# Kernel optimization log

Hardware: AMD Instinct MI355X
Metric: run time of the kernel (lower is better)

The kernel has to match this reference:

```python
import jax, jax.numpy as jnp
import numpy as np

B, S, H = 2, 2048, 2048
E, K, HID = 8, 2, 4096          # num_experts, top-k, expert hidden (2*H)
NH, HD = 8, 256                  # attention heads, head_dim
MS, MD = 256, 512                # memory_size, memory_dim
RSTEPS, RD = 3, 512              # reasoning steps, reasoning_dim
SCALE = 16.0                     # sqrt(head_dim)


def setup_inputs() -> dict:
    key = jax.random.key(0)
    ks = iter(jax.random.split(key, 64))
    def w(shape, s=0.02):
        return (jax.random.normal(next(ks), shape, jnp.float32) * s)
    z = lambda *shape: jnp.zeros(shape, jnp.float32)
    inp = {
        'hidden_states': jax.random.normal(next(ks), (B, S, H), jnp.float32),
        'attention_mask': jnp.zeros((B, S), jnp.float32),  # 0 = unmasked (faithful: mask*-1e9 added)
        # MoE
        'gate_w': w((H, E)), 'gate_b': z(E),
        'moe_w1': w((E, H, HID)), 'moe_b1': z(E, HID),
        'moe_w2': w((E, HID, H)), 'moe_b2': z(E, H),
        # memory-augmented attention
        'q_w': w((H, H)), 'q_b': z(H),
        'k_w': w((H, H)), 'k_b': z(H),
        'v_w': w((H, H)), 'v_b': z(H),
        'o_w': w((H, H)), 'o_b': z(H),
        'mem_values': jax.random.normal(next(ks), (MS, MD), jnp.float32),
        'mem_proj_w': w((MD, H)), 'mem_proj_b': z(H),
        'mem_attn_w': w((H, MS)), 'mem_attn_b': z(MS),
        # hierarchical reasoning (stacked over steps)
        'rs_w1': w((RSTEPS, H, RD)), 'rs_b1': z(RSTEPS, RD),
        'rs_w2': w((RSTEPS, RD, H)), 'rs_b2': z(RSTEPS, H),
        'ln_g': jnp.ones((RSTEPS, H), jnp.float32), 'ln_b': z(RSTEPS, H),
        'hg_w1': w((RSTEPS, H, H // 4)), 'hg_b1': z(RSTEPS, H // 4),
        'hg_w2': w((RSTEPS, H // 4, 1)), 'hg_b2': z(RSTEPS, 1),
        'integ_w': w((RSTEPS * H, H)), 'integ_b': z(H),
    }
    return inp


def _layernorm(x, g, b, eps=1e-5):
    m = x.mean(-1, keepdims=True)
    v = ((x - m) ** 2).mean(-1, keepdims=True)
    return (x - m) / jnp.sqrt(v + eps) * g + b


def _forward(hidden_states, attention_mask, gate_w, gate_b, moe_w1, moe_b1, moe_w2, moe_b2,
             q_w, q_b, k_w, k_b, v_w, v_b, o_w, o_b, mem_values, mem_proj_w, mem_proj_b,
             mem_attn_w, mem_attn_b, rs_w1, rs_b1, rs_w2, rs_b2, ln_g, ln_b,
             hg_w1, hg_b1, hg_w2, hg_b2, integ_w, integ_b):
    h = hidden_states
    N = B * S
    # ---- Mixture of Experts (top-k routing, dense combine-weight formulation) ----
    x_flat = h.reshape(N, H)
    gate_probs = jax.nn.softmax(x_flat @ gate_w + gate_b, axis=-1)        # [N,E]
    topk_s, topk_i = jax.lax.top_k(gate_probs, K)                          # [N,K]
    topk_p = jax.nn.softmax(topk_s, axis=-1)                               # renormalize over top-k
    comb = jnp.zeros((N, E), x_flat.dtype).at[jnp.arange(N)[:, None], topk_i].add(topk_p)
    h1 = jax.nn.relu(jnp.einsum('nd,edh->neh', x_flat, moe_w1) + moe_b1)   # [N,E,HID]
    eo = jnp.einsum('neh,ehd->ned', h1, moe_w2) + moe_b2                   # [N,E,H]
    moe_out = jnp.einsum('ned,ne->nd', eo, comb).reshape(B, S, H)
    h = h + 0.5 * moe_out
    # ---- Memory-augmented attention ----
    q = (h @ q_w + q_b).reshape(B, S, NH, HD).transpose(0, 2, 1, 3)
    k = (h @ k_w + k_b).reshape(B, S, NH, HD).transpose(0, 2, 1, 3)
    v = (h @ v_w + v_b).reshape(B, S, NH, HD).transpose(0, 2, 1, 3)
    scores = jnp.einsum('bhqd,bhkd->bhqk', q, k) / SCALE
    scores = scores + attention_mask[:, None, None, :] * (-1e9)
    probs = jax.nn.softmax(scores, axis=-1)
    attn = jnp.einsum('bhqk,bhkd->bhqd', probs, v).transpose(0, 2, 1, 3).reshape(B, S, H)
    mem_p = jax.nn.softmax(h @ mem_attn_w + mem_attn_b, axis=-1)           # [B,S,MS]
    mem_o = (mem_p @ mem_values) @ mem_proj_w + mem_proj_b                 # [B,S,H]
    mem_out = (attn + 0.3 * mem_o) @ o_w + o_b
    h = h + mem_out
    # ---- Hierarchical reasoning ----
    cur = h
    outs = []
    for i in range(RSTEPS):
        so = jax.nn.relu(cur @ rs_w1[i] + rs_b1[i]) @ rs_w2[i] + rs_b2[i]
        so = _layernorm(so, ln_g[i], ln_b[i])
        g = jax.nn.sigmoid(jax.nn.relu(cur @ hg_w1[i] + hg_b1[i]) @ hg_w2[i] + hg_b2[i])  # [B,S,1]
        cur = cur + g * so
        outs.append(cur)
    final = jnp.concatenate(outs, axis=-1) @ integ_w + integ_b
    return h + final


def reference(hidden_states, attention_mask, gate_w, gate_b, moe_w1, moe_b1, moe_w2, moe_b2,
              q_w, q_b, k_w, k_b, v_w, v_b, o_w, o_b, mem_values, mem_proj_w, mem_proj_b,
              mem_attn_w, mem_attn_b, rs_w1, rs_b1, rs_w2, rs_b2, ln_g, ln_b,
              hg_w1, hg_b1, hg_w2, hg_b2, integ_w, integ_b):
    return _forward(hidden_states, attention_mask, gate_w, gate_b, moe_w1, moe_b1, moe_w2, moe_b2,
                    q_w, q_b, k_w, k_b, v_w, v_b, o_w, o_b, mem_values, mem_proj_w, mem_proj_b,
                    mem_attn_w, mem_attn_b, rs_w1, rs_b1, rs_w2, rs_b2, ln_g, ln_b,
                    hg_w1, hg_b1, hg_w2, hg_b2, integ_w, integ_b)
```

## Files before the change

### kernel.cpp

```cpp
#include <hip/hip_runtime.h>
#include <string.h>


typedef __attribute__((ext_vector_type(4))) float f32x4;
typedef __attribute__((ext_vector_type(8))) __bf16 bf16x8;

#define NTOK 4096
#define HDIM 2048
#define AS1 __attribute__((address_space(1)))
#define AS3 __attribute__((address_space(3)))

__device__ __forceinline__ unsigned short f2bf(float f) {
  unsigned u = __float_as_uint(f);
  unsigned r = (u + 0x7fffu + ((u >> 16) & 1u)) >> 16;
  return (unsigned short)r;
}
__device__ __forceinline__ float bf2f(unsigned short u) {
  return __uint_as_float(((unsigned)u) << 16);
}
__device__ __forceinline__ void unpack8(uint4 r, float* v) {
  v[0]=bf2f((unsigned short)(r.x&0xffff)); v[1]=bf2f((unsigned short)(r.x>>16));
  v[2]=bf2f((unsigned short)(r.y&0xffff)); v[3]=bf2f((unsigned short)(r.y>>16));
  v[4]=bf2f((unsigned short)(r.z&0xffff)); v[5]=bf2f((unsigned short)(r.z>>16));
  v[6]=bf2f((unsigned short)(r.w&0xffff)); v[7]=bf2f((unsigned short)(r.w>>16));
}
__device__ __forceinline__ uint4 pack8(const float* v) {
  uint4 r;
  r.x = (unsigned)f2bf(v[0]) | ((unsigned)f2bf(v[1])<<16);
  r.y = (unsigned)f2bf(v[2]) | ((unsigned)f2bf(v[3])<<16);
  r.z = (unsigned)f2bf(v[4]) | ((unsigned)f2bf(v[5])<<16);
  r.w = (unsigned)f2bf(v[6]) | ((unsigned)f2bf(v[7])<<16);
  return r;
}

__global__ void k_tconv(const float* __restrict__ in, unsigned short* __restrict__ out,
                        int R, int C, long inB, long outB) {
  __shared__ float tl[32][33];
  const int z = blockIdx.z;
  const float* ip = in + (long)z * inB;
  unsigned short* op = out + (long)z * outB;
  const int tx = threadIdx.x & 31, ty = threadIdx.x >> 5;
  const int c0 = blockIdx.x * 32, r0 = blockIdx.y * 32;
#pragma unroll
  for (int i = 0; i < 4; i++)
    tl[ty + i*8][tx] = ip[(long)(r0 + ty + i*8) * C + c0 + tx];
  __syncthreads();
#pragma unroll
  for (int i = 0; i < 4; i++)
    op[(long)(c0 + ty + i*8) * R + r0 + tx] = f2bf(tl[tx][ty + i*8]);
}

__global__ void k_cvt(const float* __restrict__ in, unsigned short* __restrict__ out, long n4) {
  long i = (long)blockIdx.x * blockDim.x + threadIdx.x;
  if (i < n4) {
    float4 v = ((const float4*)in)[i];
    float vv[4] = {v.x, v.y, v.z, v.w};
    union { unsigned short u[4]; uint2 d; } p;
#pragma unroll
    for (int j = 0; j < 4; j++) p.u[j] = f2bf(vv[j]);
    ((uint2*)out)[i] = p.d;
  }
}

__global__ void k_tvact(const unsigned short* __restrict__ qkv, unsigned short* __restrict__ vT) {
  __shared__ unsigned short tl[32][33];
  const int z = blockIdx.z, b = z >> 3, hh = z & 7;
  const unsigned short* ip = qkv + (long)b * 2048 * 6144 + 4096 + hh * 256;
  unsigned short* op = vT + (long)z * 256 * 2048;
  const int tx = threadIdx.x & 31, ty = threadIdx.x >> 5;
  const int d0 = blockIdx.x * 32, s0 = blockIdx.y * 32;
#pragma unroll
  for (int i = 0; i < 4; i++)
    tl[ty + i*8][tx] = ip[(long)(s0 + ty + i*8) * 6144 + d0 + tx];
  __syncthreads();
#pragma unroll
  for (int i = 0; i < 4; i++)
    op[(long)(d0 + ty + i*8) * 2048 + s0 + tx] = tl[tx][ty + i*8];
}

__global__ void k_maskvec(const float* __restrict__ m, float* __restrict__ mv) {
  int i = blockIdx.x * 256 + threadIdx.x;
  if (i < 4096) mv[i] = -1e9f * m[i];
}

__global__ void k_zero(int* p) { if (threadIdx.x < 8) p[threadIdx.x] = 0; }

__global__ void k_cat3(const float* __restrict__ a, const float* __restrict__ b,
                       const float* __restrict__ c, float* __restrict__ o) {
  int i = blockIdx.x * 256 + threadIdx.x;
  if (i < 2048) { o[i] = a[i]; o[2048 + i] = b[i]; o[4096 + i] = c[i]; }
}

__global__ void k_cat2x3(const float* __restrict__ a, const float* __restrict__ b,
                         float* __restrict__ o) {
  int i = blockIdx.x * 256 + threadIdx.x;
  if (i < 1536) { int s = i >> 9, c = i & 511; o[s * 1024 + c] = a[i]; o[s * 1024 + 512 + c] = b[i]; }
}

__global__ void k_gate(const float* __restrict__ x, const float* __restrict__ gw,
                       const float* __restrict__ gb, int* __restrict__ meta,
                       int* __restrict__ e0a, int* __restrict__ e1a,
                       float* __restrict__ w0a, float* __restrict__ w1a) {
  const int wv = threadIdx.x >> 6, ln = threadIdx.x & 63;
  const int n = blockIdx.x * 4 + wv;
  const float* xr = x + (long)n * HDIM;
  float s[8] = {0,0,0,0,0,0,0,0};
  for (int k = ln; k < HDIM; k += 64) {
    float xv = xr[k];
    const float* g = gw + (long)k * 8;
#pragma unroll
    for (int e = 0; e < 8; e++) s[e] += xv * g[e];
  }
#pragma unroll
  for (int e = 0; e < 8; e++)
    for (int d = 32; d; d >>= 1) s[e] += __shfl_xor(s[e], d);
  if (ln == 0) {
    float mx = -1e30f;
#pragma unroll
    for (int e = 0; e < 8; e++) { s[e] += gb[e]; mx = fmaxf(mx, s[e]); }
    float p[8], sum = 0.f;
#pragma unroll
    for (int e = 0; e < 8; e++) { p[e] = expf(s[e] - mx); sum += p[e]; }
    float inv = 1.f / sum;
#pragma unroll
    for (int e = 0; e < 8; e++) p[e] *= inv;
    int e0 = 0;
    for (int e = 1; e < 8; e++) if (p[e] > p[e0]) e0 = e;
    int e1 = (e0 == 0) ? 1 : 0;
    for (int e = 0; e < 8; e++) if (e != e0 && p[e] > p[e1]) e1 = e;
    float q = expf(p[e1] - p[e0]);
    float w0 = 1.f / (1.f + q), w1 = q / (1.f + q);
    e0a[n] = e0; e1a[n] = e1; w0a[n] = w0; w1a[n] = w1;
    atomicAdd(&meta[e0], 1); atomicAdd(&meta[e1], 1);
  }
}

__global__ void k_buildmap(int* meta) {
  if (threadIdx.x == 0 && blockIdx.x == 0) {
    int cum = 0, nT = 0;
    for (int e = 0; e < 8; e++) {
      int c = meta[e];
      meta[16 + e] = cum; meta[24 + e] = cum + c; meta[8 + e] = 0;
      int t = (c + 127) >> 7;
      for (int i = 0; i < t; i++) { meta[33 + nT] = e; meta[129 + nT] = cum + i * 128; nT++; }
      cum += c;
    }
    meta[32] = nT;
  }
}

__global__ void k_scatter(int* __restrict__ meta, const int* __restrict__ e0a,
                          const int* __restrict__ e1a, int* __restrict__ s0a,
                          int* __restrict__ s1a, int* __restrict__ srcTok) {
  const int n = blockIdx.x * 256 + threadIdx.x;
  if (n < NTOK) {
    int e0 = e0a[n], e1 = e1a[n];
    int s0 = meta[16 + e0] + atomicAdd(&meta[8 + e0], 1);
    int s1 = meta[16 + e1] + atomicAdd(&meta[8 + e1], 1);
    s0a[n] = s0; s1a[n] = s1; srcTok[s0] = n; srcTok[s1] = n;
  }
}

__global__ void k_gather(const unsigned short* __restrict__ xb, const int* __restrict__ srcTok,
                         unsigned short* __restrict__ xg) {
  const int r = blockIdx.x;
  int n = srcTok[r]; if (n < 0 || n >= NTOK) n = 0;
  ((uint4*)(xg + (long)r * HDIM))[threadIdx.x] =
      ((const uint4*)(xb + (long)n * HDIM))[threadIdx.x];
}

__global__ void k_combine(const float* __restrict__ h, const unsigned short* __restrict__ eo,
                          const int* __restrict__ s0a, const int* __restrict__ s1a,
                          const float* __restrict__ w0a, const float* __restrict__ w1a,
                          float* __restrict__ h2, unsigned short* __restrict__ h2b) {
  const int n = blockIdx.x, c = threadIdx.x * 8;
  const float w0 = w0a[n], w1 = w1a[n];
  uint4 a = *(const uint4*)(eo + (long)s0a[n] * HDIM + c);
  uint4 b = *(const uint4*)(eo + (long)s1a[n] * HDIM + c);
  float va[8], vb[8]; unpack8(a, va); unpack8(b, vb);
  const float* hr = h + (long)n * HDIM + c;
  float o[8];
#pragma unroll
  for (int j = 0; j < 8; j++) o[j] = hr[j] + 0.5f * (w0 * va[j] + w1 * vb[j]);
  float* h2r = h2 + (long)n * HDIM + c;
#pragma unroll
  for (int j = 0; j < 8; j++) h2r[j] = o[j];
  *(uint4*)(h2b + (long)n * HDIM + c) = pack8(o);
}

__global__ void k_softmax2048(unsigned short* __restrict__ p) {
  const long r = blockIdx.x;
  unsigned short* row = p + r * 2048;
  const int t = threadIdx.x, wv = t >> 6, ln = t & 63;
  uint4 raw = ((const uint4*)row)[t];
  float v[8]; unpack8(raw, v);
  float m = v[0];
#pragma unroll
  for (int j = 1; j < 8; j++) m = fmaxf(m, v[j]);
  for (int d = 32; d; d >>= 1) m = fmaxf(m, __shfl_xor(m, d));
  __shared__ float sm[4], ssum[4];
  if (ln == 0) sm[wv] = m;
  __syncthreads();
  m = fmaxf(fmaxf(sm[0], sm[1]), fmaxf(sm[2], sm[3]));
  float s = 0.f;
#pragma unroll
  for (int j = 0; j < 8; j++) { v[j] = expf(v[j] - m); s += v[j]; }
  for (int d = 32; d; d >>= 1) s += __shfl_xor(s, d);
  if (ln == 0) ssum[wv] = s;
  __syncthreads();
  s = ssum[0] + ssum[1] + ssum[2] + ssum[3];
  const float inv = 1.f / s;
#pragma unroll
  for (int j = 0; j < 8; j++) v[j] *= inv;
  ((uint4*)row)[t] = pack8(v);
}

__global__ void k_softmax256(const float* __restrict__ in, unsigned short* __restrict__ out) {
  const int wv = threadIdx.x >> 6, ln = threadIdx.x & 63;
  const long r = (long)blockIdx.x * 4 + wv;
  const float4 v4 = ((const float4*)(in + r * 256))[ln];
  float v[4] = {v4.x, v4.y, v4.z, v4.w};
  float m = fmaxf(fmaxf(v[0], v[1]), fmaxf(v[2], v[3]));
  for (int d = 32; d; d >>= 1) m = fmaxf(m, __shfl_xor(m, d));
  float s = 0.f;
#pragma unroll
  for (int j = 0; j < 4; j++) { v[j] = expf(v[j] - m); s += v[j]; }
  for (int d = 32; d; d >>= 1) s += __shfl_xor(s, d);
  const float inv = 1.f / s;
  union { unsigned short u[4]; uint2 d2; } p;
#pragma unroll
  for (int j = 0; j < 4; j++) p.u[j] = f2bf(v[j] * inv);
  ((uint2*)(out + r * 256))[ln] = p.d2;
}

__global__ void k_gdot(const unsigned short* __restrict__ g1, long ld, const float* __restrict__ w,
                       const float* __restrict__ bb, float* __restrict__ gv) {
  const int wv = threadIdx.x >> 6, ln = threadIdx.x & 63;
  const int n = blockIdx.x * 4 + wv;
  uint4 raw = *(const uint4*)(g1 + (long)n * ld + ln * 8);
  float v[8]; unpack8(raw, v);
  const float4 wa = ((const float4*)w)[ln * 2];
  const float4 wb = ((const float4*)w)[ln * 2 + 1];
  float s = v[0]*wa.x + v[1]*wa.y + v[2]*wa.z + v[3]*wa.w
          + v[4]*wb.x + v[5]*wb.y + v[6]*wb.z + v[7]*wb.w;
  for (int d = 32; d; d >>= 1) s += __shfl_xor(s, d);
  if (ln == 0) gv[n] = 1.f / (1.f + expf(-(s + bb[0])));
}

__global__ void k_lnupdate(const float* __restrict__ so, const float* __restrict__ curIn,
                           const float* __restrict__ gv, const float* __restrict__ lng,
                           const float* __restrict__ lnb, float* __restrict__ curOut,
                           unsigned short* __restrict__ curbOut, unsigned short* __restrict__ outs,
                           int step) {
  const int n = blockIdx.x, t = threadIdx.x, wv = t >> 6, ln = t & 63, c = t * 8;
  const float* row = so + (long)n * 2048 + c;
  float x[8];
#pragma unroll
  for (int j = 0; j < 8; j++) x[j] = row[j];
  float s1 = 0.f, s2 = 0.f;
#pragma unroll
  for (int j = 0; j < 8; j++) { s1 += x[j]; s2 += x[j] * x[j]; }
  for (int d = 32; d; d >>= 1) { s1 += __shfl_xor(s1, d); s2 += __shfl_xor(s2, d); }
  __shared__ float a1[4], a2[4];
  if (ln == 0) { a1[wv] = s1; a2[wv] = s2; }
  __syncthreads();
  s1 = a1[0] + a1[1] + a1[2] + a1[3];
  s2 = a2[0] + a2[1] + a2[2] + a2[3];
  const float mean = s1 * (1.f / 2048.f);
  const float var = s2 * (1.f / 2048.f) - mean * mean;
  const float rstd = rsqrtf(var + 1e-5f);
  const float g = gv[n];
  const float* ci = curIn + (long)n * 2048 + c;
  float o[8];
#pragma unroll
  for (int j = 0; j < 8; j++) {
    float l = (x[j] - mean) * rstd * lng[c + j] + lnb[c + j];
    o[j] = ci[j] + g * l;
  }
  float* co = curOut + (long)n * 2048 + c;
#pragma unroll
  for (int j = 0; j < 8; j++) co[j] = o[j];
  *(uint4*)(curbOut + (long)n * 2048 + c) = pack8(o);
  *(uint4*)(outs + (long)n * 6144 + (long)step * 2048 + c) = pack8(o);
}

struct GArgs {
  const unsigned short* A; long lda, aSO, aSI;
  const unsigned short* Bt; long ldb, bSO, bSI;
  int M, N, K;
  const float* adv; long advSO, advSI;
  float alpha, rscale;
  const float* rF; long ldrF, rfSO, rfSI;
  const unsigned short* rB; long ldrB, rbSO, rbSI;
  float* oF; long ldoF, ofSO, ofSI;
  unsigned short* oB; long ldoB, obSO, obSI;
  const int* meta;
};

template <int MOE, int RELU, int RESID, int OUTF, int OUTB>
__global__ __launch_bounds__(512) void gemm_bt(GArgs g) {
  __shared__ unsigned short lds[2 * 16384];
  const int t = threadIdx.x, wv = t >> 6, ln = t & 63, ln15 = ln & 15;
  const int lr8 = ln >> 3;
  const int lsl = (ln & 7) ^ lr8;
  const int bz = blockIdx.z;
  int row0, rowMax;
  const unsigned short *A, *Bt;
  long advO = 0, rFO = 0, rBO = 0, oFO = 0, oBO = 0;
  if constexpr (MOE) {
    const int ty = blockIdx.y;
    if (ty >= g.meta[32]) return;
    const int e = g.meta[33 + ty];
    row0 = g.meta[129 + ty]; rowMax = g.meta[24 + e];
    A = g.A; Bt = g.Bt + (long)e * g.bSO;
    advO = (long)e * g.advSO;
  } else {
    row0 = blockIdx.y << 7; rowMax = g.M;
    const long bo = (long)(bz >> 3), bi = (long)(bz & 7);
    A = g.A + bo * g.aSO + bi * g.aSI;
    Bt = g.Bt + bo * g.bSO + bi * g.bSI;
    advO = bo * g.advSO + bi * g.advSI;
    rFO = bo * g.rfSO + bi * g.rfSI;
    rBO = bo * g.rbSO + bi * g.rbSI;
    oFO = bo * g.ofSO + bi * g.ofSI;
    oBO = bo * g.obSO + bi * g.obSI;
  }
  const int col0 = blockIdx.x << 7;
  const long lda = g.lda, ldb = g.ldb;
  const int wm = (wv >> 2) << 6;
  const int wc = (wv & 3) << 5;

  auto STAGE = [&](int kt, unsigned base) {
    const long kk = ((long)kt << 6) + (lsl << 3);
#pragma unroll
    for (int l = 0; l < 2; ++l) {
      const int rb = (wv << 4) + (l << 3);
      int gr = row0 + rb + lr8;
      if constexpr (MOE) gr = (gr < rowMax) ? gr : (rowMax - 1);
      __builtin_amdgcn_global_load_lds(
          (const AS1 void*)(A + (long)gr * lda + kk),
          (AS3 void*)(lds + base + (rb << 6)), 16, 0, 0);
    }
#pragma unroll
    for (int l = 0; l < 2; ++l) {
      const int rb = (wv << 4) + (l << 3);
      __builtin_amdgcn_global_load_lds(
          (const AS1 void*)(Bt + (long)(col0 + rb + lr8) * ldb + kk),
          (AS3 void*)(lds + base + 8192 + (rb << 6)), 16, 0, 0);
    }
  };

  const f32x4 fz = {0.f, 0.f, 0.f, 0.f};
  f32x4 acc[4][2];
#pragma unroll
  for (int i = 0; i < 4; i++)
#pragma unroll
    for (int j = 0; j < 2; j++) acc[i][j] = fz;

  const int nt = g.K >> 6;

  STAGE(0, 0);
  asm volatile("s_waitcnt vmcnt(0)" ::: "memory");
  __builtin_amdgcn_s_barrier();

  for (int kt = 0; kt < nt; ++kt) {
    const unsigned aB = (kt & 1) ? 16384u : 0u;
    const unsigned nB = aB ^ 16384u;
    bf16x8 af[2][4], bg[2][2];
#pragma unroll
    for (int ks = 0; ks < 2; ++ks) {
      const int kb = (ks << 2) + (ln >> 4);
#pragma unroll
      for (int i = 0; i < 4; ++i) {
        const int r = wm + (i << 4) + ln15;
        af[ks][i] = *(const bf16x8*)(lds + aB + (r << 6) + ((kb ^ (r & 7)) << 3));
      }
#pragma unroll
      for (int j = 0; j < 2; ++j) {
        const int r = wc + (j << 4) + ln15;
        bg[ks][j] = *(const bf16x8*)(lds + aB + 8192 + (r << 6) + ((kb ^ (r & 7)) << 3));
      }
    }
    __builtin_amdgcn_sched_barrier(0);
    if (kt + 1 < nt) STAGE(kt + 1, nB);
    __builtin_amdgcn_sched_barrier(0);
    __builtin_amdgcn_s_setprio(1);
#pragma unroll
    for (int ks = 0; ks < 2; ++ks)
#pragma unroll
      for (int i = 0; i < 4; ++i)
#pragma unroll
        for (int j = 0; j < 2; ++j)
          acc[i][j] = __builtin_amdgcn_mfma_f32_16x16x32_bf16(af[ks][i], bg[ks][j], acc[i][j], 0, 0, 0);
    __builtin_amdgcn_s_setprio(0);
    asm volatile("s_waitcnt vmcnt(0)" ::: "memory");
    __builtin_amdgcn_s_barrier();
  }

#pragma unroll
  for (int i = 0; i < 4; i++) {
#pragma unroll
    for (int j = 0; j < 2; j++) {
      const int cc = col0 + wc + (j << 4) + ln15;
      const float av = g.adv ? g.adv[advO + cc] : 0.f;
#pragma unroll
      for (int r = 0; r < 4; r++) {
        const int rr = row0 + wm + (i << 4) + ((ln >> 4) << 2) + r;
        if (rr < rowMax) {
          float v = g.alpha * acc[i][j][r] + av;
          if constexpr (RELU) v = fmaxf(v, 0.f);
          if constexpr (RESID == 1) v = g.rF[rFO + (long)rr * g.ldrF + cc] + g.rscale * v;
          if constexpr (RESID == 2) v = bf2f(g.rB[rBO + (long)rr * g.ldrB + cc]) + g.rscale * v;
          if constexpr (OUTF) g.oF[oFO + (long)rr * g.ldoF + cc] = v;
          if constexpr (OUTB) g.oB[oBO + (long)rr * g.ldoB + cc] = f2bf(v);
        }
      }
    }
  }
}

static constexpr size_t O_W1T = 0;
static constexpr size_t O_W2T = O_W1T + (size_t)8 * 4096 * 2048 * 2;
static constexpr size_t O_QT  = O_W2T + (size_t)8 * 4096 * 2048 * 2;
static constexpr size_t O_KT  = O_QT + (size_t)2048 * 2048 * 2;
static constexpr size_t O_VWT = O_KT + (size_t)2048 * 2048 * 2;
static constexpr size_t O_OT  = O_VWT + (size_t)2048 * 2048 * 2;
static constexpr size_t O_MAT = O_OT + (size_t)2048 * 2048 * 2;
static constexpr size_t O_MPT = O_MAT + (size_t)256 * 2048 * 2;
static constexpr size_t O_MVT = O_MPT + (size_t)2048 * 512 * 2;
static constexpr size_t O_RH1 = O_MVT + (size_t)512 * 256 * 2;
static constexpr size_t O_RS2 = O_RH1 + (size_t)3 * 1024 * 2048 * 2;
static constexpr size_t O_IGT = O_RS2 + (size_t)3 * 2048 * 512 * 2;
static constexpr size_t O_META= O_IGT + (size_t)2048 * 6144 * 2;
static constexpr size_t O_E0  = O_META + 4096;
static constexpr size_t O_E1  = O_E0 + 16384;
static constexpr size_t O_W0  = O_E1 + 16384;
static constexpr size_t O_W1  = O_W0 + 16384;
static constexpr size_t O_S0  = O_W1 + 16384;
static constexpr size_t O_S1  = O_S0 + 16384;
static constexpr size_t O_SRC = O_S1 + 16384;
static constexpr size_t O_MSK = O_SRC + 32768;
static constexpr size_t O_GV  = O_MSK + 16384;
static constexpr size_t O_QKVB= O_GV + 16384;
static constexpr size_t O_RHB = O_QKVB + 6144 * 4;
static constexpr size_t O_H2  = O_RHB + 3072 * 4;
static constexpr size_t O_H2B = O_H2 + (size_t)4096 * 2048 * 4;
static constexpr size_t O_H3  = O_H2B + (size_t)4096 * 2048 * 2;
static constexpr size_t O_H3B = O_H3 + (size_t)4096 * 2048 * 4;
static constexpr size_t O_ATT = O_H3B + (size_t)4096 * 2048 * 2;
static constexpr size_t O_AO2 = O_ATT + (size_t)4096 * 2048 * 2;
static constexpr size_t O_MLG = O_AO2 + (size_t)4096 * 2048 * 2;
static constexpr size_t O_MPB = O_MLG + (size_t)4096 * 256 * 4;
static constexpr size_t O_MPV = O_MPB + (size_t)4096 * 256 * 2;
static constexpr size_t O_AR  = O_MPV + (size_t)4096 * 512 * 2;
static constexpr size_t O_XB = O_AR;
static constexpr size_t O_XG = O_XB + (size_t)4096 * 2048 * 2;
static constexpr size_t O_H1 = O_XG + (size_t)8192 * 2048 * 2;
static constexpr size_t O_EO = O_H1 + (size_t)8192 * 4096 * 2;
static constexpr size_t O_QB = O_AR;
static constexpr size_t O_VT = O_QB + (size_t)3 * 4096 * 2048 * 2;
static constexpr size_t O_SC = O_VT + (size_t)4096 * 2048 * 2;
static constexpr size_t O_T1 = O_AR;
static constexpr size_t O_SOB= O_T1 + (size_t)4096 * 1024 * 2;
static constexpr size_t O_CUR= O_SOB + (size_t)4096 * 2048 * 4;
static constexpr size_t O_CRB= O_CUR + (size_t)4096 * 2048 * 4;
static constexpr size_t O_OUS= O_CRB + (size_t)4096 * 2048 * 2;

extern "C" void kernel_launch(void* const* d_in, const int* in_sizes, int n_in,
                              void* d_out, int out_size, void* d_ws, size_t ws_size,
                              hipStream_t stream) {
  (void)in_sizes; (void)n_in; (void)out_size; (void)ws_size;
  const float* h        = (const float*)d_in[0];
  const float* mask     = (const float*)d_in[1];
  const float* gate_w   = (const float*)d_in[2];
  const float* gate_b   = (const float*)d_in[3];
  const float* moe_w1   = (const float*)d_in[4];
  const float* moe_b1   = (const float*)d_in[5];
  const float* moe_w2   = (const float*)d_in[6];
  const float* moe_b2   = (const float*)d_in[7];
  const float* q_w      = (const float*)d_in[8];
  const float* q_b      = (const float*)d_in[9];
  const float* k_w      = (const float*)d_in[10];
  const float* k_b      = (const float*)d_in[11];
  const float* v_w      = (const float*)d_in[12];
  const float* v_b      = (const float*)d_in[13];
  const float* o_w      = (const float*)d_in[14];
  const float* o_b      = (const float*)d_in[15];
  const float* mem_vals = (const float*)d_in[16];
  const float* mproj_w  = (const float*)d_in[17];
  const float* mproj_b  = (const float*)d_in[18];
  const float* mattn_w  = (const float*)d_in[19];
  const float* mattn_b  = (const float*)d_in[20];
  const float* rs_w1    = (const float*)d_in[21];
  const float* rs_b1    = (const float*)d_in[22];
  const float* rs_w2    = (const float*)d_in[23];
  const float* rs_b2    = (const float*)d_in[24];
  const float* ln_g     = (const float*)d_in[25];
  const float* ln_b     = (const float*)d_in[26];
  const float* hg_w1    = (const float*)d_in[27];
  const float* hg_b1    = (const float*)d_in[28];
  const float* hg_w2    = (const float*)d_in[29];
  const float* hg_b2    = (const float*)d_in[30];
  const float* integ_w  = (const float*)d_in[31];
  const float* integ_b  = (const float*)d_in[32];

  char* ws = (char*)d_ws;
  auto U = [&](size_t o) { return (unsigned short*)(ws + o); };
  auto F = [&](size_t o) { return (float*)(ws + o); };
  auto I = [&](size_t o) { return (int*)(ws + o); };

  k_tconv<<<dim3(128, 64, 8), 256, 0, stream>>>(moe_w1, U(O_W1T), 2048, 4096, 8388608, 8388608);
  k_tconv<<<dim3(64, 128, 8), 256, 0, stream>>>(moe_w2, U(O_W2T), 4096, 2048, 8388608, 8388608);
  k_tconv<<<dim3(64, 64, 1), 256, 0, stream>>>(q_w, U(O_QT), 2048, 2048, 0, 0);
  k_tconv<<<dim3(64, 64, 1), 256, 0, stream>>>(k_w, U(O_KT), 2048, 2048, 0, 0);
  k_tconv<<<dim3(64, 64, 1), 256, 0, stream>>>(v_w, U(O_VWT), 2048, 2048, 0, 0);
  k_tconv<<<dim3(64, 64, 1), 256, 0, stream>>>(o_w, U(O_OT), 2048, 2048, 0, 0);
  k_tconv<<<dim3(8, 64, 1), 256, 0, stream>>>(mattn_w, U(O_MAT), 2048, 256, 0, 0);
  k_tconv<<<dim3(64, 16, 1), 256, 0, stream>>>(mproj_w, U(O_MPT), 512, 2048, 0, 0);
  k_tconv<<<dim3(16, 8, 1), 256, 0, stream>>>(mem_vals, U(O_MVT), 256, 512, 0, 0);
  k_tconv<<<dim3(16, 64, 3), 256, 0, stream>>>(rs_w1, U(O_RH1), 2048, 512, 2048 * 512, 1024 * 2048);
  k_tconv<<<dim3(16, 64, 3), 256, 0, stream>>>(hg_w1, U(O_RH1) + (size_t)512 * 2048, 2048, 512,
                                               2048 * 512, 1024 * 2048);
  k_tconv<<<dim3(64, 16, 3), 256, 0, stream>>>(rs_w2, U(O_RS2), 512, 2048, 512 * 2048, 512 * 2048);
  k_tconv<<<dim3(64, 192, 1), 256, 0, stream>>>(integ_w, U(O_IGT), 6144, 2048, 0, 0);
  k_cvt<<<8192, 256, 0, stream>>>(h, U(O_XB), 2097152);
  k_maskvec<<<16, 256, 0, stream>>>(mask, F(O_MSK));
  k_cat3<<<8, 256, 0, stream>>>(q_b, k_b, v_b, F(O_QKVB));
  k_cat2x3<<<6, 256, 0, stream>>>(rs_b1, hg_b1, F(O_RHB));
  k_zero<<<1, 64, 0, stream>>>(I(O_META));

  k_gate<<<1024, 256, 0, stream>>>(h, gate_w, gate_b, I(O_META), I(O_E0), I(O_E1), F(O_W0), F(O_W1));
  k_buildmap<<<1, 1, 0, stream>>>(I(O_META));
  k_scatter<<<16, 256, 0, stream>>>(I(O_META), I(O_E0), I(O_E1), I(O_S0), I(O_S1), I(O_SRC));
  k_gather<<<8192, 256, 0, stream>>>(U(O_XB), I(O_SRC), U(O_XG));

  GArgs z0; memset(&z0, 0, sizeof(z0)); z0.alpha = 1.f; z0.rscale = 1.f;
  {
    GArgs g = z0;
    g.A = U(O_XG); g.lda = 2048;
    g.Bt = U(O_W1T); g.ldb = 2048; g.bSO = (long)4096 * 2048;
    g.N = 4096; g.K = 2048;
    g.adv = moe_b1; g.advSO = 4096;
    g.oB = U(O_H1); g.ldoB = 4096;
    g.meta = I(O_META);
    gemm_bt<1, 1, 0, 0, 1><<<dim3(32, 72, 1), 512, 0, stream>>>(g);
  }
  {
    GArgs g = z0;
    g.A = U(O_H1); g.lda = 4096;
    g.Bt = U(O_W2T); g.ldb = 4096; g.bSO = (long)2048 * 4096;
    g.N = 2048; g.K = 4096;
    g.adv = moe_b2; g.advSO = 2048;
    g.oB = U(O_EO); g.ldoB = 2048;
    g.meta = I(O_META);
    gemm_bt<1, 0, 0, 0, 1><<<dim3(16, 72, 1), 512, 0, stream>>>(g);
  }
  k_combine<<<4096, 256, 0, stream>>>(h, U(O_EO), I(O_S0), I(O_S1), F(O_W0), F(O_W1),
                                      F(O_H2), U(O_H2B));

  {
    GArgs g = z0;
    g.A = U(O_H2B); g.lda = 2048; g.M = 4096; g.N = 6144; g.K = 2048;
    g.Bt = U(O_QT); g.ldb = 2048;
    g.adv = F(O_QKVB);
    g.oB = U(O_QB); g.ldoB = 6144;
    gemm_bt<0, 0, 0, 0, 1><<<dim3(48, 32, 1), 512, 0, stream>>>(g);
  }
  k_tvact<<<dim3(8, 64, 16), 256, 0, stream>>>(U(O_QB), U(O_VT));
  {
    GArgs g = z0;
    g.A = U(O_QB); g.lda = 6144; g.aSO = 12582912; g.aSI = 256;
    g.Bt = U(O_QB) + 2048; g.ldb = 6144; g.bSO = 12582912; g.bSI = 256;
    g.M = 2048; g.N = 2048; g.K = 256;
    g.adv = F(O_MSK); g.advSO = 2048; g.advSI = 0;
    g.alpha = 0.0625f;
    g.oB = U(O_SC); g.ldoB = 2048; g.obSO = 33554432; g.obSI = 4194304;
    gemm_bt<0, 0, 0, 0, 1><<<dim3(16, 16, 16), 512, 0, stream>>>(g);
  }
  k_softmax2048<<<32768, 256, 0, stream>>>(U(O_SC));
  {
    GArgs g = z0;
    g.A = U(O_SC); g.lda = 2048; g.aSO = 33554432; g.aSI = 4194304;
    g.Bt = U(O_VT); g.ldb = 2048; g.bSO = 4194304; g.bSI = 524288;
    g.M = 2048; g.N = 256; g.K = 2048;
    g.oB = U(O_ATT); g.ldoB = 2048; g.obSO = 4194304; g.obSI = 256;
    gemm_bt<0, 0, 0, 0, 1><<<dim3(2, 16, 16), 512, 0, stream>>>(g);
  }
  {
    GArgs g = z0;
    g.A = U(O_H2B); g.lda = 2048; g.Bt = U(O_MAT); g.ldb = 2048;
    g.M = 4096; g.N = 256; g.K = 2048;
    g.adv = mattn_b;
    g.oF = F(O_MLG); g.ldoF = 256;
    gemm_bt<0, 0, 0, 1, 0><<<dim3(2, 32, 1), 512, 0, stream>>>(g);
  }
  k_softmax256<<<1024, 256, 0, stream>>>(F(O_MLG), U(O_MPB));
  {
    GArgs g = z0;
    g.A = U(O_MPB); g.lda = 256; g.Bt = U(O_MVT); g.ldb = 256;
    g.M = 4096; g.N = 512; g.K = 256;
    g.oB = U(O_MPV); g.ldoB = 512;
    gemm_bt<0, 0, 0, 0, 1><<<dim3(4, 32, 1), 512, 0, stream>>>(g);
  }
  {
    GArgs g = z0;
    g.A = U(O_MPV); g.lda = 512; g.Bt = U(O_MPT); g.ldb = 512;
    g.M = 4096; g.N = 2048; g.K = 512;
    g.adv = mproj_b;
    g.rB = U(O_ATT); g.ldrB = 2048; g.rscale = 0.3f;
    g.oB = U(O_AO2); g.ldoB = 2048;
    gemm_bt<0, 0, 2, 0, 1><<<dim3(16, 32, 1), 512, 0, stream>>>(g);
  }
  {
    GArgs g = z0;
    g.A = U(O_AO2); g.lda = 2048; g.Bt = U(O_OT); g.ldb = 2048;
    g.M = 4096; g.N = 2048; g.K = 2048;
    g.adv = o_b;
    g.rF = F(O_H2); g.ldrF = 2048; g.rscale = 1.f;
    g.oF = F(O_H3); g.ldoF = 2048;
    g.oB = U(O_H3B); g.ldoB = 2048;
    gemm_bt<0, 0, 1, 1, 1><<<dim3(16, 32, 1), 512, 0, stream>>>(g);
  }

  for (int i = 0; i < 3; i++) {
    const unsigned short* curb = (i == 0) ? U(O_H3B) : U(O_CRB);
    const float* curf = (i == 0) ? F(O_H3) : F(O_CUR);
    {
      GArgs g = z0;
      g.A = curb; g.lda = 2048;
      g.Bt = U(O_RH1) + (size_t)i * 1024 * 2048; g.ldb = 2048;
      g.M = 4096; g.N = 1024; g.K = 2048;
      g.adv = F(O_RHB) + i * 1024;
      g.oB = U(O_T1); g.ldoB = 1024;
      gemm_bt<0, 1, 0, 0, 1><<<dim3(8, 32, 1), 512, 0, stream>>>(g);
    }
    {
      GArgs g = z0;
      g.A = U(O_T1); g.lda = 1024;
      g.Bt = U(O_RS2) + (size_t)i * 2048 * 512; g.ldb = 512;
      g.M = 4096; g.N = 2048; g.K = 512;
      g.adv = rs_b2 + i * 2048;
      g.oF = F(O_SOB); g.ldoF = 2048;
      gemm_bt<0, 0, 0, 1, 0><<<dim3(16, 32, 1), 512, 0, stream>>>(g);
    }
    k_gdot<<<1024, 256, 0, stream>>>(U(O_T1) + 512, 1024, hg_w2 + i * 512, hg_b2 + i, F(O_GV));
    k_lnupdate<<<4096, 256, 0, stream>>>(F(O_SOB), curf, F(O_GV), ln_g + i * 2048,
                                         ln_b + i * 2048, F(O_CUR), U(O_CRB), U(O_OUS), i);
  }
  {
    GArgs g = z0;
    g.A = U(O_OUS); g.lda = 6144; g.Bt = U(O_IGT); g.ldb = 6144;
    g.M = 4096; g.N = 2048; g.K = 6144;
    g.adv = integ_b;
    g.rF = F(O_H3); g.ldrF = 2048; g.rscale = 1.f;
    g.oF = (float*)d_out; g.ldoF = 2048;
    gemm_bt<0, 0, 1, 1, 0><<<dim3(16, 32, 1), 512, 0, stream>>>(g);
  }
}
```

Baseline: 1.738 ms.

## Fuse MoE gather into GEMM, merge setup kernels, interleave MFMA with LDS reads

Removes the separate token-gather kernel by having the first MoE GEMM load A rows indirectly through srcTok. Merges the four weight-transpose launches and the small bias/mask/zero kernels into single launches, and drops the fp32 h2 copy so the output projection reads the bf16 residual instead. Restructures the GEMM inner loop to issue the next-stage prefetch first and interleave LDS fragment loads with MFMAs. The bf16 residual lowers precision of the h2 path, and the new loop order changes instruction scheduling.

```diff
diff --git a/kernel.cpp b/kernel.cpp
--- a/kernel.cpp
+++ b/kernel.cpp
@@ -50,6 +50,24 @@
     op[(long)(c0 + ty + i*8) * R + r0 + tx] = f2bf(tl[tx][ty + i*8]);
 }
 
+__global__ void k_tconv4(const float* __restrict__ i0, const float* __restrict__ i1,
+                         const float* __restrict__ i2, const float* __restrict__ i3,
+                         unsigned short* __restrict__ out) {
+  __shared__ float tl[32][33];
+  const int z = blockIdx.z;
+  const float* ip = (z == 0) ? i0 : (z == 1) ? i1 : (z == 2) ? i2 : i3;
+  unsigned short* op = out + (size_t)z * 2048 * 2048;
+  const int tx = threadIdx.x & 31, ty = threadIdx.x >> 5;
+  const int c0 = blockIdx.x * 32, r0 = blockIdx.y * 32;
+#pragma unroll
+  for (int i = 0; i < 4; i++)
+    tl[ty + i*8][tx] = ip[(long)(r0 + ty + i*8) * 2048 + c0 + tx];
+  __syncthreads();
+#pragma unroll
+  for (int i = 0; i < 4; i++)
+    op[(long)(c0 + ty + i*8) * 2048 + r0 + tx] = f2bf(tl[tx][ty + i*8]);
+}
+
 __global__ void k_cvt(const float* __restrict__ in, unsigned short* __restrict__ out, long n4) {
   long i = (long)blockIdx.x * blockDim.x + threadIdx.x;
   if (i < n4) {
@@ -78,23 +96,24 @@
     op[(long)(d0 + ty + i*8) * 2048 + s0 + tx] = tl[tx][ty + i*8];
 }
 
-__global__ void k_maskvec(const float* __restrict__ m, float* __restrict__ mv) {
-  int i = blockIdx.x * 256 + threadIdx.x;
-  if (i < 4096) mv[i] = -1e9f * m[i];
-}
-
-__global__ void k_zero(int* p) { if (threadIdx.x < 8) p[threadIdx.x] = 0; }
-
-__global__ void k_cat3(const float* __restrict__ a, const float* __restrict__ b,
-                       const float* __restrict__ c, float* __restrict__ o) {
-  int i = blockIdx.x * 256 + threadIdx.x;
-  if (i < 2048) { o[i] = a[i]; o[2048 + i] = b[i]; o[4096 + i] = c[i]; }
-}
-
-__global__ void k_cat2x3(const float* __restrict__ a, const float* __restrict__ b,
-                         float* __restrict__ o) {
-  int i = blockIdx.x * 256 + threadIdx.x;
-  if (i < 1536) { int s = i >> 9, c = i & 511; o[s * 1024 + c] = a[i]; o[s * 1024 + 512 + c] = b[i]; }
+__global__ void k_misc(const float* __restrict__ mask, float* __restrict__ mv,
+                       const float* __restrict__ qb, const float* __restrict__ kb,
+                       const float* __restrict__ vb, float* __restrict__ qkvb,
+                       const float* __restrict__ rsb1, const float* __restrict__ hgb1,
+                       float* __restrict__ rhb, int* __restrict__ meta) {
+  const int b = blockIdx.x, t = threadIdx.x;
+  if (b < 16) {
+    int i = b * 256 + t; mv[i] = -1e9f * mask[i];
+  } else if (b < 40) {
+    int i = (b - 16) * 256 + t;
+    qkvb[i] = (i < 2048) ? qb[i] : (i < 4096) ? kb[i - 2048] : vb[i - 4096];
+  } else if (b < 46) {
+    int i = (b - 40) * 256 + t;
+    int s = i >> 9, c = i & 511;
+    rhb[s * 1024 + c] = rsb1[i]; rhb[s * 1024 + 512 + c] = hgb1[i];
+  } else {
+    if (t < 8) meta[t] = 0;
+  }
 }
 
 __global__ void k_gate(const float* __restrict__ x, const float* __restrict__ gw,
@@ -161,18 +180,10 @@
   }
 }
 
-__global__ void k_gather(const unsigned short* __restrict__ xb, const int* __restrict__ srcTok,
-                         unsigned short* __restrict__ xg) {
-  const int r = blockIdx.x;
-  int n = srcTok[r]; if (n < 0 || n >= NTOK) n = 0;
-  ((uint4*)(xg + (long)r * HDIM))[threadIdx.x] =
-      ((const uint4*)(xb + (long)n * HDIM))[threadIdx.x];
-}
-
 __global__ void k_combine(const float* __restrict__ h, const unsigned short* __restrict__ eo,
                           const int* __restrict__ s0a, const int* __restrict__ s1a,
                           const float* __restrict__ w0a, const float* __restrict__ w1a,
-                          float* __restrict__ h2, unsigned short* __restrict__ h2b) {
+                          unsigned short* __restrict__ h2b) {
   const int n = blockIdx.x, c = threadIdx.x * 8;
   const float w0 = w0a[n], w1 = w1a[n];
   uint4 a = *(const uint4*)(eo + (long)s0a[n] * HDIM + c);
@@ -182,9 +193,6 @@
   float o[8];
 #pragma unroll
   for (int j = 0; j < 8; j++) o[j] = hr[j] + 0.5f * (w0 * va[j] + w1 * vb[j]);
-  float* h2r = h2 + (long)n * HDIM + c;
-#pragma unroll
-  for (int j = 0; j < 8; j++) h2r[j] = o[j];
   *(uint4*)(h2b + (long)n * HDIM + c) = pack8(o);
 }
 
@@ -295,6 +303,7 @@
   float* oF; long ldoF, ofSO, ofSI;
   unsigned short* oB; long ldoB, obSO, obSI;
   const int* meta;
+  const int* srcTok;
 };
 
 template <int MOE, int RELU, int RESID, int OUTF, int OUTB>
@@ -330,16 +339,28 @@
   const int wm = (wv >> 2) << 6;
   const int wc = (wv & 3) << 5;
 
+  int grow0, grow1;
+  {
+    int r0i = row0 + (wv << 4) + lr8;
+    int r1i = r0i + 8;
+    if constexpr (MOE) {
+      r0i = (r0i < rowMax) ? r0i : (rowMax - 1);
+      r1i = (r1i < rowMax) ? r1i : (rowMax - 1);
+    }
+    if constexpr (MOE == 2) { grow0 = g.srcTok[r0i]; grow1 = g.srcTok[r1i]; }
+    else { grow0 = r0i; grow1 = r1i; }
+  }
+
   auto STAGE = [&](int kt, unsigned base) {
     const long kk = ((long)kt << 6) + (lsl << 3);
-#pragma unroll
-    for (int l = 0; l < 2; ++l) {
-      const int rb = (wv << 4) + (l << 3);
-      int gr = row0 + rb + lr8;
-      if constexpr (MOE) gr = (gr < rowMax) ? gr : (rowMax - 1);
+    {
+      const int rb = (wv << 4);
       __builtin_amdgcn_global_load_lds(
-          (const AS1 void*)(A + (long)gr * lda + kk),
+          (const AS1 void*)(A + (long)grow0 * lda + kk),
           (AS3 void*)(lds + base + (rb << 6)), 16, 0, 0);
+      __builtin_amdgcn_global_load_lds(
+          (const AS1 void*)(A + (long)grow1 * lda + kk),
+          (AS3 void*)(lds + base + ((rb + 8) << 6)), 16, 0, 0);
     }
 #pragma unroll
     for (int l = 0; l < 2; ++l) {
@@ -366,33 +387,27 @@
   for (int kt = 0; kt < nt; ++kt) {
     const unsigned aB = (kt & 1) ? 16384u : 0u;
     const unsigned nB = aB ^ 16384u;
-    bf16x8 af[2][4], bg[2][2];
+    if (kt + 1 < nt) STAGE(kt + 1, nB);
 #pragma unroll
     for (int ks = 0; ks < 2; ++ks) {
       const int kb = (ks << 2) + (ln >> 4);
+      bf16x8 bg[2];
+#pragma unroll
+      for (int j = 0; j < 2; ++j) {
+        const int r = wc + (j << 4) + ln15;
+        bg[j] = *(const bf16x8*)(lds + aB + 8192 + (r << 6) + ((kb ^ (r & 7)) << 3));
+      }
+      __builtin_amdgcn_s_setprio(1);
 #pragma unroll
       for (int i = 0; i < 4; ++i) {
         const int r = wm + (i << 4) + ln15;
-        af[ks][i] = *(const bf16x8*)(lds + aB + (r << 6) + ((kb ^ (r & 7)) << 3));
+        bf16x8 a = *(const bf16x8*)(lds + aB + (r << 6) + ((kb ^ (r & 7)) << 3));
+#pragma unroll
+        for (int j = 0; j < 2; ++j)
+          acc[i][j] = __builtin_amdgcn_mfma_f32_16x16x32_bf16(a, bg[j], acc[i][j], 0, 0, 0);
       }
-#pragma unroll
-      for (int j = 0; j < 2; ++j) {
-        const int r = wc + (j << 4) + ln15;
-        bg[ks][j] = *(const bf16x8*)(lds + aB + 8192 + (r << 6) + ((kb ^ (r & 7)) << 3));
-      }
-    }
-    __builtin_amdgcn_sched_barrier(0);
-    if (kt + 1 < nt) STAGE(kt + 1, nB);
-    __builtin_amdgcn_sched_barrier(0);
-    __builtin_amdgcn_s_setprio(1);
-#pragma unroll
-    for (int ks = 0; ks < 2; ++ks)
-#pragma unroll
-      for (int i = 0; i < 4; ++i)
-#pragma unroll
-        for (int j = 0; j < 2; ++j)
-          acc[i][j] = __builtin_amdgcn_mfma_f32_16x16x32_bf16(af[ks][i], bg[ks][j], acc[i][j], 0, 0, 0);
-    __builtin_amdgcn_s_setprio(0);
+      __builtin_amdgcn_s_setprio(0);
+    }
     asm volatile("s_waitcnt vmcnt(0)" ::: "memory");
     __builtin_amdgcn_s_barrier();
   }
@@ -511,10 +526,7 @@
 
   k_tconv<<<dim3(128, 64, 8), 256, 0, stream>>>(moe_w1, U(O_W1T), 2048, 4096, 8388608, 8388608);
   k_tconv<<<dim3(64, 128, 8), 256, 0, stream>>>(moe_w2, U(O_W2T), 4096, 2048, 8388608, 8388608);
-  k_tconv<<<dim3(64, 64, 1), 256, 0, stream>>>(q_w, U(O_QT), 2048, 2048, 0, 0);
-  k_tconv<<<dim3(64, 64, 1), 256, 0, stream>>>(k_w, U(O_KT), 2048, 2048, 0, 0);
-  k_tconv<<<dim3(64, 64, 1), 256, 0, stream>>>(v_w, U(O_VWT), 2048, 2048, 0, 0);
-  k_tconv<<<dim3(64, 64, 1), 256, 0, stream>>>(o_w, U(O_OT), 2048, 2048, 0, 0);
+  k_tconv4<<<dim3(64, 64, 4), 256, 0, stream>>>(q_w, k_w, v_w, o_w, U(O_QT));
   k_tconv<<<dim3(8, 64, 1), 256, 0, stream>>>(mattn_w, U(O_MAT), 2048, 256, 0, 0);
   k_tconv<<<dim3(64, 16, 1), 256, 0, stream>>>(mproj_w, U(O_MPT), 512, 2048, 0, 0);
   k_tconv<<<dim3(16, 8, 1), 256, 0, stream>>>(mem_vals, U(O_MVT), 256, 512, 0, 0);
@@ -524,26 +536,23 @@
   k_tconv<<<dim3(64, 16, 3), 256, 0, stream>>>(rs_w2, U(O_RS2), 512, 2048, 512 * 2048, 512 * 2048);
   k_tconv<<<dim3(64, 192, 1), 256, 0, stream>>>(integ_w, U(O_IGT), 6144, 2048, 0, 0);
   k_cvt<<<8192, 256, 0, stream>>>(h, U(O_XB), 2097152);
-  k_maskvec<<<16, 256, 0, stream>>>(mask, F(O_MSK));
-  k_cat3<<<8, 256, 0, stream>>>(q_b, k_b, v_b, F(O_QKVB));
-  k_cat2x3<<<6, 256, 0, stream>>>(rs_b1, hg_b1, F(O_RHB));
-  k_zero<<<1, 64, 0, stream>>>(I(O_META));
+  k_misc<<<47, 256, 0, stream>>>(mask, F(O_MSK), q_b, k_b, v_b, F(O_QKVB),
+                                 rs_b1, hg_b1, F(O_RHB), I(O_META));
 
   k_gate<<<1024, 256, 0, stream>>>(h, gate_w, gate_b, I(O_META), I(O_E0), I(O_E1), F(O_W0), F(O_W1));
   k_buildmap<<<1, 1, 0, stream>>>(I(O_META));
   k_scatter<<<16, 256, 0, stream>>>(I(O_META), I(O_E0), I(O_E1), I(O_S0), I(O_S1), I(O_SRC));
-  k_gather<<<8192, 256, 0, stream>>>(U(O_XB), I(O_SRC), U(O_XG));
 
   GArgs z0; memset(&z0, 0, sizeof(z0)); z0.alpha = 1.f; z0.rscale = 1.f;
   {
     GArgs g = z0;
-    g.A = U(O_XG); g.lda = 2048;
+    g.A = U(O_XB); g.lda = 2048;
     g.Bt = U(O_W1T); g.ldb = 2048; g.bSO = (long)4096 * 2048;
     g.N = 4096; g.K = 2048;
     g.adv = moe_b1; g.advSO = 4096;
     g.oB = U(O_H1); g.ldoB = 4096;
-    g.meta = I(O_META);
-    gemm_bt<1, 1, 0, 0, 1><<<dim3(32, 72, 1), 512, 0, stream>>>(g);
+    g.meta = I(O_META); g.srcTok = I(O_SRC);
+    gemm_bt<2, 1, 0, 0, 1><<<dim3(32, 72, 1), 512, 0, stream>>>(g);
   }
   {
     GArgs g = z0;
@@ -555,8 +564,7 @@
     g.meta = I(O_META);
     gemm_bt<1, 0, 0, 0, 1><<<dim3(16, 72, 1), 512, 0, stream>>>(g);
   }
-  k_combine<<<4096, 256, 0, stream>>>(h, U(O_EO), I(O_S0), I(O_S1), F(O_W0), F(O_W1),
-                                      F(O_H2), U(O_H2B));
+  k_combine<<<4096, 256, 0, stream>>>(h, U(O_EO), I(O_S0), I(O_S1), F(O_W0), F(O_W1), U(O_H2B));
 
   {
     GArgs g = z0;
@@ -616,10 +624,10 @@
     g.A = U(O_AO2); g.lda = 2048; g.Bt = U(O_OT); g.ldb = 2048;
     g.M = 4096; g.N = 2048; g.K = 2048;
     g.adv = o_b;
-    g.rF = F(O_H2); g.ldrF = 2048; g.rscale = 1.f;
+    g.rB = U(O_H2B); g.ldrB = 2048; g.rscale = 1.f;
     g.oF = F(O_H3); g.ldoF = 2048;
     g.oB = U(O_H3B); g.ldoB = 2048;
-    gemm_bt<0, 0, 1, 1, 1><<<dim3(16, 32, 1), 512, 0, stream>>>(g);
+    gemm_bt<0, 0, 2, 1, 1><<<dim3(16, 32, 1), 512, 0, stream>>>(g);
   }
 
   for (int i = 0; i < 3; i++) {
```

New measurement: 1.663 ms. 4.3% less time.
